# Kernel tuning notes

Hardware: AMD Instinct MI355X
Metric: run time of the kernel (lower is better)

The kernel has to match this reference:

```python
import jax, jax.numpy as jnp
import numpy as np

N, H, W = 32, 768, 768


def setup_inputs() -> dict:
    key = jax.random.key(0)
    k1, k2 = jax.random.split(key)
    logits = jax.random.normal(k1, (N, 2, H, W), dtype=jnp.float32)
    targets = jax.random.randint(k2, (N, H, W), 0, 2, dtype=jnp.int64)
    return {"logits": logits, "targets": targets}


def _topk_mask(vals, k):
    # Boolean mask selecting, per row, the k[i] largest entries of vals[i, :].
    # rank r of each element under descending sort; keep rank < k.
    order = jnp.argsort(-vals, axis=1)            # (n, L) indices, descending
    ranks = jnp.argsort(order, axis=1)            # (n, L) rank of each position
    return ranks < k[:, None]


def reference(logits, targets):
    n = logits.shape[0]
    logits = logits.reshape(n, 2, -1)             # (n, 2, L)
    t = targets.reshape(n, -1)                    # (n, L) in {0,1}

    # per-pixel cross entropy, reduction='none'
    logp = jax.nn.log_softmax(logits, axis=1)     # (n, 2, L)
    ce = -jnp.take_along_axis(logp, t[:, None, :], axis=1)[:, 0, :]  # (n, L)

    # hard mining masks (no-grad region in original)
    pos_loss = jnp.where(t < 1, 0.0, ce)          # zero where target == 0
    neg_loss = jnp.where(t > 1, 0.0, ce)          # (never zeroed for binary t)
    pos_count = jnp.sum(t != 0, axis=1)           # (n,)
    neg_count = jnp.sum((1 - t) != 0, axis=1)     # (n,)
    min_count = jnp.minimum(pos_count, neg_count) # (n,)

    mask = _topk_mask(pos_loss, min_count) | _topk_mask(neg_loss, min_count)
    grad_masks = jax.lax.stop_gradient(mask.astype(jnp.int64))  # values in {0,1}

    # Faithful to torch `ce_loss[grad_masks]`: integer advanced indexing picks
    # ROWS 0/1 of ce, giving shape (n, L, L); its mean equals the mean of
    # rowmean(ce)[grad_masks] -- computed without materializing (n, L, L).
    rowmean = ce.mean(axis=1)                     # (n,)
    return rowmean[grad_masks].mean()
```

## Files before the change

kernel.cpp:

```cpp
#include <hip/hip_runtime.h>

constexpr int NROWS     = 32;
constexpr int HW        = 768 * 768;
constexpr int CHUNKS    = 64;
constexpr int CHUNK_PIX = HW / CHUNKS;
constexpr int NB        = 4096;
constexpr int THREADS   = 256;

constexpr size_t OFF_ROWPART = 0;
constexpr size_t OFF_ROWC    = 8192;
constexpr size_t OFF_ROWTOT  = 8448;
constexpr size_t OFF_HIST    = 10240;
constexpr size_t OFF_POSHIST = OFF_HIST + (size_t)NROWS * NB * 4;
constexpr size_t WS_USED     = OFF_POSHIST + (size_t)NROWS * NB * 4;

__global__ __launch_bounds__(THREADS) void ce_hist_kernel(
    const float* __restrict__ logits, const int* __restrict__ targets,
    float* __restrict__ rowpart,
    unsigned* __restrict__ hist, unsigned* __restrict__ poshist)
{
    __shared__ unsigned lh[NB];
    __shared__ float    redf[THREADS / 64];

    const int blk   = blockIdx.x;
    const int row   = blk / CHUNKS;
    const int chunk = blk % CHUNKS;

    for (int b = threadIdx.x; b < NB; b += THREADS) lh[b] = 0u;
    __syncthreads();

    const float* x0 = logits + (size_t)row * 2 * HW + (size_t)chunk * CHUNK_PIX;
    const float* x1 = x0 + HW;
    const int*   tp = targets + (size_t)row * HW + (size_t)chunk * CHUNK_PIX;

    constexpr float L2E = 1.4426950408889634f;
    float lsum = 0.f;

    for (int p = threadIdx.x * 4; p < CHUNK_PIX; p += THREADS * 4) {
        float4 a0 = *(const float4*)(x0 + p);
        float4 a1 = *(const float4*)(x1 + p);
        int4   t4 = *(const int4*)(tp + p);
        const float* v0 = (const float*)&a0;
        const float* v1 = (const float*)&a1;
        const int*   tv = (const int*)&t4;
#pragma unroll
        for (int j = 0; j < 4; ++j) {
            const unsigned t = (unsigned)tv[j];
            float u = (v0[j] - v1[j]) * L2E;
            u = __uint_as_float(__float_as_uint(u) ^ (t << 31));
            const float e2  = exp2f(-fabsf(u));
            const float ce2 = fmaxf(-u, 0.f) + __log2f(1.f + e2);
            lsum += ce2;
            unsigned key = __float_as_uint(ce2) >> 19;
            if (key > NB - 1) key = NB - 1;
            atomicAdd(&lh[key], 1u | (t << 16));
        }
    }

    for (int o = 32; o > 0; o >>= 1) lsum += __shfl_down(lsum, o);
    const int wid  = threadIdx.x >> 6;
    const int lane = threadIdx.x & 63;
    if (lane == 0) redf[wid] = lsum;
    __syncthreads();

    if (threadIdx.x == 0) {
        float s = 0.f;
        for (int w = 0; w < THREADS / 64; ++w) s += redf[w];
        rowpart[row * CHUNKS + chunk] = s;
    }

    for (int b = threadIdx.x; b < NB; b += THREADS) {
        const unsigned v = lh[b];
        if (v) {
            atomicAdd(&hist[(size_t)row * NB + b], v & 0xFFFFu);
            const unsigned hi = v >> 16;
            if (hi) atomicAdd(&poshist[(size_t)row * NB + b], hi);
        }
    }
}

__global__ __launch_bounds__(256) void select_kernel(
    const unsigned* __restrict__ hist, const unsigned* __restrict__ poshist,
    const float* __restrict__ rowpart,
    double* __restrict__ rowC, double* __restrict__ rowtot)
{
    __shared__ unsigned lh[NB];
    __shared__ unsigned lph[NB];
    __shared__ unsigned segsum[256];
    __shared__ unsigned segpsum[256];
    __shared__ unsigned segsuf[256];
    __shared__ int      s_tb;
    __shared__ unsigned s_cgt;
    __shared__ unsigned s_posgt;
    __shared__ unsigned s_pos;

    const int row = blockIdx.x;
    const int tid = threadIdx.x;

    for (int b = tid; b < NB; b += 256) {
        lh[b]  = hist[(size_t)row * NB + b];
        lph[b] = poshist[(size_t)row * NB + b];
    }
    __syncthreads();

    const int base = NB - 16 * (tid + 1);
    unsigned ssum = 0u, psum = 0u;
#pragma unroll
    for (int j = 0; j < 16; ++j) { ssum += lh[base + j]; psum += lph[base + j]; }
    segsum[tid]  = ssum;
    segpsum[tid] = psum;
    __syncthreads();

    if (tid == 0) {
        unsigned c = 0u, pc = 0u;
        for (int t = 0; t < 256; ++t) { segsuf[t] = c; c += segsum[t]; pc += segpsum[t]; }
        s_pos   = pc;
        s_tb    = -1;
        s_cgt   = 0u;
        s_posgt = 0u;
    }
    __syncthreads();

    const unsigned pos = s_pos;
    const unsigned k   = min(pos, (unsigned)HW - pos);

    if (k > 0) {
        const unsigned above = segsuf[tid];
        if (above < k && above + ssum >= k) {
            unsigned cum = above;
            for (int b = base + 15; b >= base; --b) {
                const unsigned nv = cum + lh[b];
                if (nv >= k) { s_tb = b; s_cgt = cum; break; }
                cum = nv;
            }
        }
    }
    __syncthreads();

    const int tb = s_tb;
    unsigned mypos = 0u;
    if (tb >= 0) {
#pragma unroll
        for (int j = 0; j < 16; ++j) {
            const int b = base + j;
            if (b > tb) mypos += lph[b];
        }
    }
    for (int o = 32; o > 0; o >>= 1) mypos += __shfl_down(mypos, o);
    if ((tid & 63) == 0) atomicAdd(&s_posgt, mypos);
    __syncthreads();

    if (tid == 0) {
        double Cr = 0.0;
        if (k > 0 && tb >= 0) {
            const unsigned rneed = k - s_cgt;
            const unsigned hb = lh[tb], phb = lph[tb];
            const double P = (double)s_posgt +
                             (hb ? (double)rneed * (double)phb / (double)hb : 0.0);
            Cr = 2.0 * (double)k - P;
        }
        rowC[row] = Cr;
        double s = 0.0;
        for (int c = 0; c < CHUNKS; ++c) s += (double)rowpart[row * CHUNKS + c];
        rowtot[row] = s;
    }
}

__global__ void final_kernel(const double* __restrict__ rowC,
                             const double* __restrict__ rowtot,
                             float* __restrict__ out)
{
    constexpr double LN2 = 0.6931471805599453;
    double C = 0.0;
    for (int r = 0; r < NROWS; ++r) C += rowC[r];
    const double nL = (double)NROWS * (double)HW;
    const double r0 = rowtot[0] / (double)HW * LN2;
    const double r1 = rowtot[1] / (double)HW * LN2;
    out[0] = (float)(((nL - C) * r0 + C * r1) / nL);
}

extern "C" void kernel_launch(void* const* d_in, const int* in_sizes, int n_in,
                              void* d_out, int out_size, void* d_ws, size_t ws_size,
                              hipStream_t stream) {
    const float* logits  = (const float*)d_in[0];
    const int*   targets = (const int*)d_in[1];
    float*       out     = (float*)d_out;
    char*        ws      = (char*)d_ws;

    hipMemsetAsync(ws + OFF_HIST, 0, WS_USED - OFF_HIST, stream);

    ce_hist_kernel<<<NROWS * CHUNKS, THREADS, 0, stream>>>(
        logits, targets,
        (float*)(ws + OFF_ROWPART),
        (unsigned*)(ws + OFF_HIST), (unsigned*)(ws + OFF_POSHIST));

    select_kernel<<<NROWS, 256, 0, stream>>>(
        (const unsigned*)(ws + OFF_HIST), (const unsigned*)(ws + OFF_POSHIST),
        (const float*)(ws + OFF_ROWPART),
        (double*)(ws + OFF_ROWC), (double*)(ws + OFF_ROWTOT));

    final_kernel<<<1, 1, 0, stream>>>(
        (const double*)(ws + OFF_ROWC), (const double*)(ws + OFF_ROWTOT), out);
}
```

Baseline: 56.30 us.

## Pack count and positive histograms into 64-bit atomics and unroll pixel loads

New measurement: 61.79 us. +9.7%, slower.

```diff
diff --git a/kernel.cpp b/kernel.cpp
--- a/kernel.cpp
+++ b/kernel.cpp
@@ -10,14 +10,31 @@
 constexpr size_t OFF_ROWPART = 0;
 constexpr size_t OFF_ROWC    = 8192;
 constexpr size_t OFF_ROWTOT  = 8448;
-constexpr size_t OFF_HIST    = 10240;
-constexpr size_t OFF_POSHIST = OFF_HIST + (size_t)NROWS * NB * 4;
-constexpr size_t WS_USED     = OFF_POSHIST + (size_t)NROWS * NB * 4;
+constexpr size_t OFF_HIST64  = 16384;
+constexpr size_t WS_USED     = OFF_HIST64 + (size_t)NROWS * NB * 8;
+
+__global__ __launch_bounds__(256) void zero_hist_kernel(ulonglong2* __restrict__ h)
+{
+    h[(size_t)blockIdx.x * 256 + threadIdx.x] = ulonglong2{0ull, 0ull};
+}
+
+__device__ __forceinline__ void px(float a0, float a1, unsigned t,
+                                   float& lsum, unsigned* lh)
+{
+    constexpr float L2E = 1.4426950408889634f;
+    float u = (a0 - a1) * L2E;
+    u = __uint_as_float(__float_as_uint(u) ^ (t << 31));
+    const float e2  = exp2f(-fabsf(u));
+    const float ce2 = fmaxf(-u, 0.f) + __log2f(1.f + e2);
+    lsum += ce2;
+    unsigned key = __float_as_uint(ce2) >> 19;
+    if (key > NB - 1) key = NB - 1;
+    atomicAdd(&lh[key], 1u | (t << 16));
+}
 
 __global__ __launch_bounds__(THREADS) void ce_hist_kernel(
     const float* __restrict__ logits, const int* __restrict__ targets,
-    float* __restrict__ rowpart,
-    unsigned* __restrict__ hist, unsigned* __restrict__ poshist)
+    float* __restrict__ rowpart, unsigned long long* __restrict__ hist)
 {
     __shared__ unsigned lh[NB];
     __shared__ float    redf[THREADS / 64];
@@ -33,28 +50,38 @@
     const float* x1 = x0 + HW;
     const int*   tp = targets + (size_t)row * HW + (size_t)chunk * CHUNK_PIX;
 
-    constexpr float L2E = 1.4426950408889634f;
     float lsum = 0.f;
 
-    for (int p = threadIdx.x * 4; p < CHUNK_PIX; p += THREADS * 4) {
-        float4 a0 = *(const float4*)(x0 + p);
-        float4 a1 = *(const float4*)(x1 + p);
-        int4   t4 = *(const int4*)(tp + p);
-        const float* v0 = (const float*)&a0;
-        const float* v1 = (const float*)&a1;
-        const int*   tv = (const int*)&t4;
-#pragma unroll
-        for (int j = 0; j < 4; ++j) {
-            const unsigned t = (unsigned)tv[j];
-            float u = (v0[j] - v1[j]) * L2E;
-            u = __uint_as_float(__float_as_uint(u) ^ (t << 31));
-            const float e2  = exp2f(-fabsf(u));
-            const float ce2 = fmaxf(-u, 0.f) + __log2f(1.f + e2);
-            lsum += ce2;
-            unsigned key = __float_as_uint(ce2) >> 19;
-            if (key > NB - 1) key = NB - 1;
-            atomicAdd(&lh[key], 1u | (t << 16));
-        }
+#pragma unroll
+    for (int it = 0; it < 4; ++it) {
+        const int p = it * (THREADS * 8) + threadIdx.x * 8;
+        const float4 a0 = *(const float4*)(x0 + p);
+        const float4 b0 = *(const float4*)(x0 + p + 4);
+        const float4 a1 = *(const float4*)(x1 + p);
+        const float4 b1 = *(const float4*)(x1 + p + 4);
+        const int4   t0 = *(const int4*)(tp + p);
+        const int4   t1 = *(const int4*)(tp + p + 4);
+        const float* va0 = (const float*)&a0;
+        const float* vb0 = (const float*)&b0;
+        const float* va1 = (const float*)&a1;
+        const float* vb1 = (const float*)&b1;
+        const int*   tv0 = (const int*)&t0;
+        const int*   tv1 = (const int*)&t1;
+#pragma unroll
+        for (int j = 0; j < 4; ++j) px(va0[j], va1[j], (unsigned)tv0[j], lsum, lh);
+#pragma unroll
+        for (int j = 0; j < 4; ++j) px(vb0[j], vb1[j], (unsigned)tv1[j], lsum, lh);
+    }
+    {
+        const int p = 4 * (THREADS * 8) + threadIdx.x * 4;
+        const float4 a0 = *(const float4*)(x0 + p);
+        const float4 a1 = *(const float4*)(x1 + p);
+        const int4   t0 = *(const int4*)(tp + p);
+        const float* va0 = (const float*)&a0;
+        const float* va1 = (const float*)&a1;
+        const int*   tv0 = (const int*)&t0;
+#pragma unroll
+        for (int j = 0; j < 4; ++j) px(va0[j], va1[j], (unsigned)tv0[j], lsum, lh);
     }
 
     for (int o = 32; o > 0; o >>= 1) lsum += __shfl_down(lsum, o);
@@ -72,15 +99,15 @@
     for (int b = threadIdx.x; b < NB; b += THREADS) {
         const unsigned v = lh[b];
         if (v) {
-            atomicAdd(&hist[(size_t)row * NB + b], v & 0xFFFFu);
-            const unsigned hi = v >> 16;
-            if (hi) atomicAdd(&poshist[(size_t)row * NB + b], hi);
+            const unsigned long long add =
+                ((unsigned long long)(v & 0xFFFFu) << 32) | (v >> 16);
+            atomicAdd(&hist[(size_t)row * NB + b], add);
         }
     }
 }
 
 __global__ __launch_bounds__(256) void select_kernel(
-    const unsigned* __restrict__ hist, const unsigned* __restrict__ poshist,
+    const unsigned long long* __restrict__ hist,
     const float* __restrict__ rowpart,
     double* __restrict__ rowC, double* __restrict__ rowtot)
 {
@@ -98,8 +125,9 @@
     const int tid = threadIdx.x;
 
     for (int b = tid; b < NB; b += 256) {
-        lh[b]  = hist[(size_t)row * NB + b];
-        lph[b] = poshist[(size_t)row * NB + b];
+        const unsigned long long v = hist[(size_t)row * NB + b];
+        lh[b]  = (unsigned)(v >> 32);
+        lph[b] = (unsigned)(v & 0xFFFFFFFFu);
     }
     __syncthreads();
 
@@ -187,15 +215,16 @@
     float*       out     = (float*)d_out;
     char*        ws      = (char*)d_ws;
 
-    hipMemsetAsync(ws + OFF_HIST, 0, WS_USED - OFF_HIST, stream);
+    zero_hist_kernel<<<NROWS * NB * 8 / (256 * 16), 256, 0, stream>>>(
+        (ulonglong2*)(ws + OFF_HIST64));
 
     ce_hist_kernel<<<NROWS * CHUNKS, THREADS, 0, stream>>>(
         logits, targets,
         (float*)(ws + OFF_ROWPART),
-        (unsigned*)(ws + OFF_HIST), (unsigned*)(ws + OFF_POSHIST));
+        (unsigned long long*)(ws + OFF_HIST64));
 
     select_kernel<<<NROWS, 256, 0, stream>>>(
-        (const unsigned*)(ws + OFF_HIST), (const unsigned*)(ws + OFF_POSHIST),
+        (const unsigned long long*)(ws + OFF_HIST64),
         (const float*)(ws + OFF_ROWPART),
         (double*)(ws + OFF_ROWC), (double*)(ws + OFF_ROWTOT));
 
```

## Skip CE math outside rows 0-1, bin raw logit margin, pack histograms

Applied to the files above, without the earlier changes.

After: 59.10 us. 1.05x slower.

```diff
diff --git a/kernel.cpp b/kernel.cpp
--- a/kernel.cpp
+++ b/kernel.cpp
@@ -10,21 +10,24 @@
 constexpr size_t OFF_ROWPART = 0;
 constexpr size_t OFF_ROWC    = 8192;
 constexpr size_t OFF_ROWTOT  = 8448;
-constexpr size_t OFF_HIST    = 10240;
-constexpr size_t OFF_POSHIST = OFF_HIST + (size_t)NROWS * NB * 4;
-constexpr size_t WS_USED     = OFF_POSHIST + (size_t)NROWS * NB * 4;
+constexpr size_t OFF_HIST64  = 16384;
+constexpr size_t HIST_BYTES  = (size_t)NROWS * NB * 8;
+
+__global__ __launch_bounds__(256) void zero_kernel(ulonglong2* __restrict__ h)
+{
+    h[(size_t)blockIdx.x * 256 + threadIdx.x] = ulonglong2{0ull, 0ull};
+}
 
 __global__ __launch_bounds__(THREADS) void ce_hist_kernel(
     const float* __restrict__ logits, const int* __restrict__ targets,
-    float* __restrict__ rowpart,
-    unsigned* __restrict__ hist, unsigned* __restrict__ poshist)
+    float* __restrict__ rowpart, unsigned long long* __restrict__ hist)
 {
     __shared__ unsigned lh[NB];
     __shared__ float    redf[THREADS / 64];
 
     const int blk   = blockIdx.x;
-    const int row   = blk / CHUNKS;
-    const int chunk = blk % CHUNKS;
+    const int row   = blk >> 6;
+    const int chunk = blk & 63;
 
     for (int b = threadIdx.x; b < NB; b += THREADS) lh[b] = 0u;
     __syncthreads();
@@ -32,27 +35,29 @@
     const float* x0 = logits + (size_t)row * 2 * HW + (size_t)chunk * CHUNK_PIX;
     const float* x1 = x0 + HW;
     const int*   tp = targets + (size_t)row * HW + (size_t)chunk * CHUNK_PIX;
-
-    constexpr float L2E = 1.4426950408889634f;
+    const bool needsum = (row < 2);
+
     float lsum = 0.f;
 
-    for (int p = threadIdx.x * 4; p < CHUNK_PIX; p += THREADS * 4) {
-        float4 a0 = *(const float4*)(x0 + p);
-        float4 a1 = *(const float4*)(x1 + p);
-        int4   t4 = *(const int4*)(tp + p);
+#pragma unroll 3
+    for (int it = 0; it < 9; ++it) {
+        const int p = it * (THREADS * 4) + threadIdx.x * 4;
+        const float4 a0 = *(const float4*)(x0 + p);
+        const float4 a1 = *(const float4*)(x1 + p);
+        const int4   t4 = *(const int4*)(tp + p);
         const float* v0 = (const float*)&a0;
         const float* v1 = (const float*)&a1;
         const int*   tv = (const int*)&t4;
 #pragma unroll
         for (int j = 0; j < 4; ++j) {
-            const unsigned t = (unsigned)tv[j];
-            float u = (v0[j] - v1[j]) * L2E;
-            u = __uint_as_float(__float_as_uint(u) ^ (t << 31));
-            const float e2  = exp2f(-fabsf(u));
-            const float ce2 = fmaxf(-u, 0.f) + __log2f(1.f + e2);
-            lsum += ce2;
-            unsigned key = __float_as_uint(ce2) >> 19;
-            if (key > NB - 1) key = NB - 1;
+            const unsigned t  = (unsigned)tv[j];
+            const unsigned ub = __float_as_uint(v0[j] - v1[j]) ^ (t << 31);
+            if (needsum) {
+                const float w = __uint_as_float(ub) * 1.4426950408889634f;
+                lsum += fmaxf(-w, 0.f) + __log2f(1.f + exp2f(-fabsf(w)));
+            }
+            const unsigned m   = (unsigned)((int)ub >> 31) | 0x80000000u;
+            const unsigned key = (ub ^ m) >> 20;
             atomicAdd(&lh[key], 1u | (t << 16));
         }
     }
@@ -72,15 +77,14 @@
     for (int b = threadIdx.x; b < NB; b += THREADS) {
         const unsigned v = lh[b];
         if (v) {
-            atomicAdd(&hist[(size_t)row * NB + b], v & 0xFFFFu);
-            const unsigned hi = v >> 16;
-            if (hi) atomicAdd(&poshist[(size_t)row * NB + b], hi);
+            atomicAdd(&hist[(size_t)row * NB + b],
+                      ((unsigned long long)(v & 0xFFFFu) << 32) | (v >> 16));
         }
     }
 }
 
 __global__ __launch_bounds__(256) void select_kernel(
-    const unsigned* __restrict__ hist, const unsigned* __restrict__ poshist,
+    const unsigned long long* __restrict__ hist,
     const float* __restrict__ rowpart,
     double* __restrict__ rowC, double* __restrict__ rowtot)
 {
@@ -88,22 +92,24 @@
     __shared__ unsigned lph[NB];
     __shared__ unsigned segsum[256];
     __shared__ unsigned segpsum[256];
-    __shared__ unsigned segsuf[256];
+    __shared__ unsigned segpre[256];
+    __shared__ unsigned redp[4];
     __shared__ int      s_tb;
-    __shared__ unsigned s_cgt;
-    __shared__ unsigned s_posgt;
+    __shared__ unsigned s_cbefore;
     __shared__ unsigned s_pos;
 
     const int row = blockIdx.x;
     const int tid = threadIdx.x;
 
     for (int b = tid; b < NB; b += 256) {
-        lh[b]  = hist[(size_t)row * NB + b];
-        lph[b] = poshist[(size_t)row * NB + b];
-    }
-    __syncthreads();
-
-    const int base = NB - 16 * (tid + 1);
+        const unsigned long long v = hist[(size_t)row * NB + b];
+        lh[b]  = (unsigned)(v >> 32);
+        lph[b] = (unsigned)(v & 0xFFFFFFFFu);
+    }
+    if (tid == 0) { s_tb = -1; s_cbefore = 0u; }
+    __syncthreads();
+
+    const int base = tid * 16;
     unsigned ssum = 0u, psum = 0u;
 #pragma unroll
     for (int j = 0; j < 16; ++j) { ssum += lh[base + j]; psum += lph[base + j]; }
@@ -113,11 +119,8 @@
 
     if (tid == 0) {
         unsigned c = 0u, pc = 0u;
-        for (int t = 0; t < 256; ++t) { segsuf[t] = c; c += segsum[t]; pc += segpsum[t]; }
-        s_pos   = pc;
-        s_tb    = -1;
-        s_cgt   = 0u;
-        s_posgt = 0u;
+        for (int t = 0; t < 256; ++t) { segpre[t] = c; c += segsum[t]; pc += segpsum[t]; }
+        s_pos = pc;
     }
     __syncthreads();
 
@@ -125,12 +128,13 @@
     const unsigned k   = min(pos, (unsigned)HW - pos);
 
     if (k > 0) {
-        const unsigned above = segsuf[tid];
-        if (above < k && above + ssum >= k) {
-            unsigned cum = above;
-            for (int b = base + 15; b >= base; --b) {
+        const unsigned cbeg = segpre[tid];
+        if (cbeg < k && cbeg + ssum >= k) {
+            unsigned cum = cbeg;
+            for (int j = 0; j < 16; ++j) {
+                const int b = base + j;
                 const unsigned nv = cum + lh[b];
-                if (nv >= k) { s_tb = b; s_cgt = cum; break; }
+                if (nv >= k) { s_tb = b; s_cbefore = cum; break; }
                 cum = nv;
             }
         }
@@ -138,24 +142,25 @@
     __syncthreads();
 
     const int tb = s_tb;
-    unsigned mypos = 0u;
+    unsigned myp = 0u;
     if (tb >= 0) {
 #pragma unroll
         for (int j = 0; j < 16; ++j) {
             const int b = base + j;
-            if (b > tb) mypos += lph[b];
-        }
-    }
-    for (int o = 32; o > 0; o >>= 1) mypos += __shfl_down(mypos, o);
-    if ((tid & 63) == 0) atomicAdd(&s_posgt, mypos);
+            if (b < tb) myp += lph[b];
+        }
+    }
+    for (int o = 32; o > 0; o >>= 1) myp += __shfl_down(myp, o);
+    if ((tid & 63) == 0) redp[tid >> 6] = myp;
     __syncthreads();
 
     if (tid == 0) {
         double Cr = 0.0;
         if (k > 0 && tb >= 0) {
-            const unsigned rneed = k - s_cgt;
+            const unsigned posb  = redp[0] + redp[1] + redp[2] + redp[3];
+            const unsigned rneed = k - s_cbefore;
             const unsigned hb = lh[tb], phb = lph[tb];
-            const double P = (double)s_posgt +
+            const double P = (double)posb +
                              (hb ? (double)rneed * (double)phb / (double)hb : 0.0);
             Cr = 2.0 * (double)k - P;
         }
@@ -187,15 +192,16 @@
     float*       out     = (float*)d_out;
     char*        ws      = (char*)d_ws;
 
-    hipMemsetAsync(ws + OFF_HIST, 0, WS_USED - OFF_HIST, stream);
+    zero_kernel<<<(int)(HIST_BYTES / (256 * 16)), 256, 0, stream>>>(
+        (ulonglong2*)(ws + OFF_HIST64));
 
     ce_hist_kernel<<<NROWS * CHUNKS, THREADS, 0, stream>>>(
         logits, targets,
         (float*)(ws + OFF_ROWPART),
-        (unsigned*)(ws + OFF_HIST), (unsigned*)(ws + OFF_POSHIST));
+        (unsigned long long*)(ws + OFF_HIST64));
 
     select_kernel<<<NROWS, 256, 0, stream>>>(
-        (const unsigned*)(ws + OFF_HIST), (const unsigned*)(ws + OFF_POSHIST),
+        (const unsigned long long*)(ws + OFF_HIST64),
         (const float*)(ws + OFF_ROWPART),
         (double*)(ws + OFF_ROWC), (double*)(ws + OFF_ROWTOT));
 
```
